# Kernel optimization log

Hardware: AMD Instinct MI355X
Metric: run time of the kernel (lower is better)

The kernel has to match this reference:

```python
import jax, jax.numpy as jnp
import numpy as np

B, T, D, H, C = 256, 128, 1, 2048, 10


def _xavier(key, shape):
    fan_out, fan_in = shape
    std = float(np.sqrt(2.0 / (fan_in + fan_out)))
    return jax.random.normal(key, shape, dtype=jnp.float32) * std


def setup_inputs() -> dict:
    key = jax.random.key(0)
    kx, kU, kW, kV = jax.random.split(key, 4)
    return {
        "x": jax.random.normal(kx, (B, T), dtype=jnp.float32),
        "U": _xavier(kU, (H, D)),
        "W": _xavier(kW, (H, H)),
        "V": _xavier(kV, (C, H)),
        "bh": jnp.zeros((H,), dtype=jnp.float32),
        "bp": jnp.zeros((C,), dtype=jnp.float32),
    }


def reference(x, U, W, V, bh, bp):
    # x: [B, T]; per-step input x[:, t:t+1] -> [B, 1] (input_dim == 1)
    xs = jnp.swapaxes(x, 0, 1)[:, :, None]  # [T, B, 1]

    def step(h, x_t):
        # h: [B, H]; x_t: [B, 1]
        h_new = jnp.tanh(x_t @ U.T + h @ W.T + bh)
        return h_new, None

    h0 = jnp.zeros((x.shape[0], H), dtype=x.dtype)
    h_last, _ = jax.lax.scan(step, h0, xs)
    output = h_last @ V.T + bp  # [B, C]
    return (h_last, output)
```

## Files before the change

kernel.cpp:

```cpp
#include <hip/hip_runtime.h>
#include <cmath>


#define B_ 256
#define T_ 128
#define H_ 2048
#define C_ 10

typedef _Float16 half_t;
typedef _Float16 half8 __attribute__((ext_vector_type(8)));
typedef _Float16 half4v __attribute__((ext_vector_type(4)));
typedef float floatx4 __attribute__((ext_vector_type(4)));
typedef unsigned long long u64;
typedef unsigned long long u64x2 __attribute__((ext_vector_type(2)));

#define BUF_U64 131072
#define NSLOT 127

#define FLAG_DWORDS (128 * 8 * 32 * 32)

__device__ __forceinline__ float fast_tanh(float v) {
    return 1.0f - 2.0f / (__expf(2.0f * v) + 1.0f);
}

__device__ __forceinline__ void publish_u64(u64* p, u64 v) {
    u64 old = __hip_atomic_exchange(p, v, __ATOMIC_RELAXED,
                                    __HIP_MEMORY_SCOPE_AGENT);
    asm volatile("" :: "v"(old));
}

template <int ROT>
__device__ __forceinline__ size_t slot_base(int s) {
    return ROT ? (size_t)s * BUF_U64
               : (size_t)((s + 1) & 1) * BUF_U64;
}

template <int ROT>
__global__ void __launch_bounds__(512, 2) rnn_persist(
    const float* __restrict__ x,
    const float* __restrict__ U,
    const float* __restrict__ W,
    const float* __restrict__ bh,
    const float* __restrict__ V,
    const float* __restrict__ bp,
    half_t* __restrict__ hbase,
    float* __restrict__ hf32,
    float* __restrict__ outp,
    unsigned* __restrict__ flags)
{
    const int tid  = threadIdx.x;
    const int wave = tid >> 6, lane = tid & 63;
    const int quad = lane >> 4, lq = lane & 15;
    const int id   = blockIdx.x;
    const int g    = id & 7;
    const int C    = id >> 3;
    const int m0   = g * 32;
    const int n0   = C * 64;

    half8 Bw[8][4];
#pragma unroll
    for (int kk = 0; kk < 8; ++kk) {
#pragma unroll
        for (int nt = 0; nt < 4; ++nt) {
            const int gn = n0 + nt * 16 + lq;
            const int k0 = wave * 256 + kk * 32 + quad * 8;
            const float4 w0 = *(const float4*)&W[(size_t)gn * H_ + k0];
            const float4 w1 = *(const float4*)&W[(size_t)gn * H_ + k0 + 4];
            const float wv[8] = {w0.x, w0.y, w0.z, w0.w, w1.x, w1.y, w1.z, w1.w};
            half8 hw;
#pragma unroll
            for (int j = 0; j < 8; ++j) hw[j] = (half_t)wv[j];
            Bw[kk][nt] = hw;
        }
    }

    const int mtO = wave & 1, ntO = wave >> 1;
    const float uvO = U[n0 + ntO * 16 + lq];
    const float bvO = bh[n0 + ntO * 16 + lq];

    __shared__ floatx4 red[2][8][4][64];
    __shared__ __align__(16) float Tr[8][16][20];
    __shared__ float xs[T_][32];

    for (int i = tid; i < 32 * T_; i += 512) {
        const int r = i & 31, tt = i >> 5;
        xs[tt][r] = x[(size_t)(m0 + r) * T_ + tt];
    }
    __syncthreads();

    const int prow = (tid >> 8) * 16 + ((tid >> 1) & 15);
    const int pcol = ((tid >> 7) & 1) * 32 + ((tid >> 5) & 3) * 8 + (tid & 1) * 4;
    const size_t slab = (size_t)g * 16384;
    const size_t pdst = slab + (size_t)C * 512 + tid;
    const size_t cbase = slab + (size_t)wave * 2048 + (size_t)lane * 2;

    const int sigma = mtO * 256 + (ntO >> 1) * 128
                    + ((ntO & 1) * 2 + (quad >> 1)) * 32 + lq * 2 + (quad & 1);
    const size_t pdst_o = slab + (size_t)C * 512 + sigma;

    unsigned* myflag_base = flags + ((size_t)g * 32 + C) * 32;
    const unsigned* pollp = flags + ((size_t)g * 32 + wave * 4 + (lane & 3)) * 32;

    {
        const float xb = xs[0][prow];
        half4v hv;
#pragma unroll
        for (int j = 0; j < 4; ++j) {
            const int n = n0 + pcol + j;
            hv[j] = (half_t)fast_tanh(xb * U[n] + bh[n]);
        }
        publish_u64((u64*)hbase + slot_base<ROT>(0) + pdst,
                    __builtin_bit_cast(u64, hv));
    }
    __syncthreads();
    if (tid == 0)
        __hip_atomic_fetch_add(myflag_base, 1u, __ATOMIC_RELAXED,
                               __HIP_MEMORY_SCOPE_AGENT);

    for (int t = 1; t < T_; ++t) {
        const u64* pw = (const u64*)hbase + slot_base<ROT>(t - 1) + cbase;
        u64* pout     = (u64*)hbase + slot_base<ROT>(t);

        {
            const unsigned* fp = pollp + (size_t)(t - 1) * (8 * 32 * 32);
            while (true) {
                const unsigned v = __hip_atomic_load(fp, __ATOMIC_RELAXED,
                                                     __HIP_MEMORY_SCOPE_AGENT);
                if (__all(v >= 1u)) break;
                __builtin_amdgcn_s_sleep(1);
            }
            asm volatile("" ::: "memory");
        }

        floatx4 acc[2][4] = {};

        u64 rl[8], rh[8];
        auto issue = [&](int f) {
            const u64* q = pw + (size_t)((f >> 2) * 512 + ((f >> 1) & 1) * 256
                                         + (f & 1) * 128);
            if (ROT) {
                const u64x2 v = *(const u64x2*)q;
                rl[f & 7] = v.x;
                rh[f & 7] = v.y;
            } else {
                rl[f & 7] = __hip_atomic_load(q, __ATOMIC_RELAXED,
                                              __HIP_MEMORY_SCOPE_AGENT);
                rh[f & 7] = __hip_atomic_load(q + 1, __ATOMIC_RELAXED,
                                              __HIP_MEMORY_SCOPE_AGENT);
            }
        };
#pragma unroll
        for (int f = 0; f < 8; ++f) issue(f);
#pragma unroll
        for (int f = 0; f < 16; ++f) {
            const int cp = f >> 2, mt = (f >> 1) & 1, kc = f & 1;
            const int kk = cp * 2 + kc;
            u64x2 bits; bits.x = rl[f & 7]; bits.y = rh[f & 7];
            const half8 av = __builtin_bit_cast(half8, bits);
            if (f + 8 < 16) issue(f + 8);
            acc[mt][0] = __builtin_amdgcn_mfma_f32_16x16x32_f16(av, Bw[kk][0], acc[mt][0], 0, 0, 0);
            acc[mt][1] = __builtin_amdgcn_mfma_f32_16x16x32_f16(av, Bw[kk][1], acc[mt][1], 0, 0, 0);
            acc[mt][2] = __builtin_amdgcn_mfma_f32_16x16x32_f16(av, Bw[kk][2], acc[mt][2], 0, 0, 0);
            acc[mt][3] = __builtin_amdgcn_mfma_f32_16x16x32_f16(av, Bw[kk][3], acc[mt][3], 0, 0, 0);
        }

#pragma unroll
        for (int mt = 0; mt < 2; ++mt)
#pragma unroll
            for (int nt = 0; nt < 4; ++nt)
                red[mt][wave][nt][lane] = acc[mt][nt];
        __syncthreads();

        {
            float xr[4];
#pragma unroll
            for (int r = 0; r < 4; ++r) xr[r] = xs[t][mtO * 16 + quad * 4 + r];
            floatx4 s = red[mtO][0][ntO][lane];
#pragma unroll
            for (int ww = 1; ww < 8; ++ww) s += red[mtO][ww][ntO][lane];
#pragma unroll
            for (int r = 0; r < 4; ++r) {
                const float pre = s[r] + xr[r] * uvO + bvO;
                Tr[wave][quad * 4 + r][lq] = fast_tanh(pre);
            }
            const float4 fr = *(const float4*)&Tr[wave][lq][quad * 4];

            if (t < T_ - 1) {
                half4v hv;
                hv[0] = (half_t)fr.x; hv[1] = (half_t)fr.y;
                hv[2] = (half_t)fr.z; hv[3] = (half_t)fr.w;
                publish_u64(pout + pdst_o, __builtin_bit_cast(u64, hv));
                __syncthreads();
                if (tid == 0)
                    __hip_atomic_fetch_add(
                        myflag_base + (size_t)t * (8 * 32 * 32), 1u,
                        __ATOMIC_RELAXED, __HIP_MEMORY_SCOPE_AGENT);
            } else {
                float* fd = hf32 + (size_t)(m0 + mtO * 16 + lq) * H_
                          + n0 + ntO * 16 + quad * 4;
                *(float4*)fd = make_float4(fr.x, fr.y, fr.z, fr.w);
                __syncthreads();
                if (tid < 32 * C_) {
                    const int r = tid & 31, c = tid >> 5;
                    float sacc = (C == 0) ? bp[c] : 0.0f;
                    const float* vr = V + (size_t)c * H_ + n0;
#pragma unroll 8
                    for (int n = 0; n < 64; ++n)
                        sacc += Tr[(n >> 4) * 2 + (r >> 4)][r & 15][n & 15] * vr[n];
                    atomicAdd(&outp[(size_t)(m0 + r) * C_ + c], sacc);
                }
            }
        }
    }
}

extern "C" void kernel_launch(void* const* d_in, const int* in_sizes, int n_in,
                              void* d_out, int out_size, void* d_ws, size_t ws_size,
                              hipStream_t stream) {
    const float* x  = (const float*)d_in[0];
    const float* U  = (const float*)d_in[1];
    const float* W  = (const float*)d_in[2];
    const float* V  = (const float*)d_in[3];
    const float* bh = (const float*)d_in[4];
    const float* bp = (const float*)d_in[5];

    float* out_h = (float*)d_out;
    float* outp  = out_h + (size_t)B_ * H_;

    unsigned* flags = (unsigned*)d_ws;
    half_t* hbase = (half_t*)((char*)d_ws + (size_t)4 * 1024 * 1024);

    const size_t need = (size_t)(4 + NSLOT) * 1024 * 1024;
    const int rot = ws_size >= need;

    hipMemsetAsync(flags, 0, FLAG_DWORDS * sizeof(unsigned), stream);
    hipMemsetAsync(outp, 0, (size_t)B_ * C_ * sizeof(float), stream);

    if (rot)
        rnn_persist<1><<<dim3(256), dim3(512), 0, stream>>>(
            x, U, W, bh, V, bp, hbase, out_h, outp, flags);
    else
        rnn_persist<0><<<dim3(256), dim3(512), 0, stream>>>(
            x, U, W, bh, V, bp, hbase, out_h, outp, flags);
}
```

Measured before the change: 587.1 us.

## Replace block barrier before flag publish with per-wave drain and counter

In the rotating-buffer path, each wave now drains its own outstanding memory ops and bumps the step flag itself, instead of the whole block hitting a barrier and one thread bumping it. Consumers poll until the counter reaches 8 (one per wave). The reduction scratch buffer is double-buffered by step parity, so the barrier that used to follow the publish is no longer needed to keep next-step writes from overwriting data still being read. This cuts a block-wide barrier from the critical step-to-step path, at the cost of eight atomics per flag instead of one and twice the shared memory for the reduction buffer.

```diff
diff --git a/kernel.cpp b/kernel.cpp
--- a/kernel.cpp
+++ b/kernel.cpp
@@ -27,6 +27,12 @@
     u64 old = __hip_atomic_exchange(p, v, __ATOMIC_RELAXED,
                                     __HIP_MEMORY_SCOPE_AGENT);
     asm volatile("" :: "v"(old));
+}
+
+__device__ __forceinline__ void wave_drain() {
+    __builtin_amdgcn_sched_barrier(0);
+    __builtin_amdgcn_s_waitcnt(0);
+    __builtin_amdgcn_sched_barrier(0);
 }
 
 template <int ROT>
@@ -78,7 +84,7 @@
     const float uvO = U[n0 + ntO * 16 + lq];
     const float bvO = bh[n0 + ntO * 16 + lq];
 
-    __shared__ floatx4 red[2][8][4][64];
+    __shared__ floatx4 red[2][2][8][4][64];
     __shared__ __align__(16) float Tr[8][16][20];
     __shared__ float xs[T_][32];
 
@@ -101,6 +107,8 @@
     unsigned* myflag_base = flags + ((size_t)g * 32 + C) * 32;
     const unsigned* pollp = flags + ((size_t)g * 32 + wave * 4 + (lane & 3)) * 32;
 
+    const unsigned TH = ROT ? 8u : 1u;
+
     {
         const float xb = xs[0][prow];
         half4v hv;
@@ -112,10 +120,17 @@
         publish_u64((u64*)hbase + slot_base<ROT>(0) + pdst,
                     __builtin_bit_cast(u64, hv));
     }
-    __syncthreads();
-    if (tid == 0)
-        __hip_atomic_fetch_add(myflag_base, 1u, __ATOMIC_RELAXED,
-                               __HIP_MEMORY_SCOPE_AGENT);
+    if (ROT) {
+        wave_drain();
+        if (lane == 0)
+            __hip_atomic_fetch_add(myflag_base, 1u, __ATOMIC_RELAXED,
+                                   __HIP_MEMORY_SCOPE_AGENT);
+    } else {
+        __syncthreads();
+        if (tid == 0)
+            __hip_atomic_fetch_add(myflag_base, 1u, __ATOMIC_RELAXED,
+                                   __HIP_MEMORY_SCOPE_AGENT);
+    }
 
     for (int t = 1; t < T_; ++t) {
         const u64* pw = (const u64*)hbase + slot_base<ROT>(t - 1) + cbase;
@@ -126,7 +141,7 @@
             while (true) {
                 const unsigned v = __hip_atomic_load(fp, __ATOMIC_RELAXED,
                                                      __HIP_MEMORY_SCOPE_AGENT);
-                if (__all(v >= 1u)) break;
+                if (__all(v >= TH)) break;
                 __builtin_amdgcn_s_sleep(1);
             }
             asm volatile("" ::: "memory");
@@ -168,16 +183,16 @@
         for (int mt = 0; mt < 2; ++mt)
 #pragma unroll
             for (int nt = 0; nt < 4; ++nt)
-                red[mt][wave][nt][lane] = acc[mt][nt];
+                red[t & 1][mt][wave][nt][lane] = acc[mt][nt];
         __syncthreads();
 
         {
             float xr[4];
 #pragma unroll
             for (int r = 0; r < 4; ++r) xr[r] = xs[t][mtO * 16 + quad * 4 + r];
-            floatx4 s = red[mtO][0][ntO][lane];
-#pragma unroll
-            for (int ww = 1; ww < 8; ++ww) s += red[mtO][ww][ntO][lane];
+            floatx4 s = red[t & 1][mtO][0][ntO][lane];
+#pragma unroll
+            for (int ww = 1; ww < 8; ++ww) s += red[t & 1][mtO][ww][ntO][lane];
 #pragma unroll
             for (int r = 0; r < 4; ++r) {
                 const float pre = s[r] + xr[r] * uvO + bvO;
@@ -190,11 +205,19 @@
                 hv[0] = (half_t)fr.x; hv[1] = (half_t)fr.y;
                 hv[2] = (half_t)fr.z; hv[3] = (half_t)fr.w;
                 publish_u64(pout + pdst_o, __builtin_bit_cast(u64, hv));
-                __syncthreads();
-                if (tid == 0)
-                    __hip_atomic_fetch_add(
-                        myflag_base + (size_t)t * (8 * 32 * 32), 1u,
-                        __ATOMIC_RELAXED, __HIP_MEMORY_SCOPE_AGENT);
+                if (ROT) {
+                    wave_drain();
+                    if (lane == 0)
+                        __hip_atomic_fetch_add(
+                            myflag_base + (size_t)t * (8 * 32 * 32), 1u,
+                            __ATOMIC_RELAXED, __HIP_MEMORY_SCOPE_AGENT);
+                } else {
+                    __syncthreads();
+                    if (tid == 0)
+                        __hip_atomic_fetch_add(
+                            myflag_base + (size_t)t * (8 * 32 * 32), 1u,
+                            __ATOMIC_RELAXED, __HIP_MEMORY_SCOPE_AGENT);
+                }
             } else {
                 float* fd = hf32 + (size_t)(m0 + mtO * 16 + lq) * H_
                           + n0 + ntO * 16 + quad * 4;
@@ -228,7 +251,7 @@
     float* outp  = out_h + (size_t)B_ * H_;
 
     unsigned* flags = (unsigned*)d_ws;
-    half_t* hbase = (half_t*)((char*)d_ws + (size_t)4 * 1024 * 1024);
+    half_t* hbase   = (half_t*)((char*)d_ws + (size_t)4 * 1024 * 1024);
 
     const size_t need = (size_t)(4 + NSLOT) * 1024 * 1024;
     const int rot = ws_size >= need;
```

After: 728.2 us. +24.0%, slower.
